# Optimization experiments

Hardware: AMD Instinct MI355X
Metric: run time of the kernel (lower is better)

Reference implementation:

```python
import jax, jax.numpy as jnp
import numpy as np

NP_, NA_, NS_ = 4096, 4096, 1
E_ = 131072
DIN, DOUT, H = 256, 64, 4
SLOPE = 0.2  # leaky relu negative slope


def _leaky(x):
    return jnp.where(x >= 0, x, SLOPE * x)


def setup_inputs() -> dict:
    key = jax.random.key(0)
    ks = iter(jax.random.split(key, 64))
    inp = {}
    inp['feat_P'] = jax.random.normal(next(ks), (NP_, DIN), jnp.float32)
    inp['feat_A'] = jax.random.normal(next(ks), (NA_, DIN), jnp.float32)
    inp['feat_state'] = jax.random.normal(next(ks), (NS_, DIN), jnp.float32)
    for name in ['P', 'A', 'p2p', 'p2a', 'a2p', 'a2a', 'p2s', 'a2s', 'in']:
        inp['W_' + name] = jax.random.normal(next(ks), (DOUT * H, DIN), jnp.float32) / np.sqrt(DIN)
        inp['b_' + name] = jax.random.normal(next(ks), (DOUT * H,), jnp.float32) * 0.01
    for name in ['p2p', 'p2a', 'a2p', 'a2a', 'p2s', 'a2s']:
        inp['att_%s_src' % name] = jax.random.normal(next(ks), (1, H, DOUT), jnp.float32) * 0.1
        inp['att_%s_dst' % name] = jax.random.normal(next(ks), (1, H, DOUT), jnp.float32) * 0.1
    for name, ns, nd in [('p2p', NP_, NP_), ('p2a', NP_, NA_), ('a2p', NA_, NP_), ('a2a', NA_, NA_)]:
        inp['e_%s_src' % name] = jax.random.randint(next(ks), (E_,), 0, ns, jnp.int32)
        inp['e_%s_dst' % name] = jax.random.randint(next(ks), (E_,), 0, nd, jnp.int32)
    inp['e_p2s_src'] = jnp.arange(NP_, dtype=jnp.int32)
    inp['e_p2s_dst'] = jnp.zeros((NP_,), jnp.int32)
    inp['e_a2s_src'] = jnp.arange(NA_, dtype=jnp.int32)
    inp['e_a2s_dst'] = jnp.zeros((NA_,), jnp.int32)
    return inp


def _msg_agg(feat_src, W, b, att_s, att_d, Wh_dst, src, dst, n_dst):
    # per-edge lossy_u_mul_e with comm_loss == 0 (noise branch dead):
    # gather src features, per-edge linear, per-edge softmax over HEADS (torch Softmax(dim=1)).
    h = feat_src[src]                                    # [E, DIN]
    Wh = (h @ W.T + b).reshape(-1, H, DOUT)              # [E, H, D]
    a_s = jnp.sum(Wh * att_s, axis=-1, keepdims=True)    # [E, H, 1]
    a_d = jnp.sum(Wh_dst[dst] * att_d, axis=-1, keepdims=True)
    attn = jax.nn.softmax(_leaky(a_s + a_d), axis=1)     # softmax over heads, as in original
    return jax.ops.segment_sum(Wh * attn, dst, num_segments=n_dst)


def _edge_softmax_agg(Wh_src, att_s, Wh_state, att_d, src, dst, n_dst):
    # dgl edge_softmax: destination-grouped stable softmax over incoming edges.
    a_s = jnp.sum(Wh_src * att_s, axis=-1, keepdims=True)[src]    # [E, H, 1]
    a_d = jnp.sum(Wh_state * att_d, axis=-1, keepdims=True)[dst]  # [E, H, 1]
    e = _leaky(a_s + a_d)
    m = jax.ops.segment_max(e, dst, num_segments=n_dst)
    ex = jnp.exp(e - m[dst])
    den = jax.ops.segment_sum(ex, dst, num_segments=n_dst)
    a = ex / den[dst]
    return jax.ops.segment_sum(Wh_src[src] * a, dst, num_segments=n_dst)


def reference(feat_P, feat_A, feat_state,
              W_P, b_P, W_A, b_A, W_p2p, b_p2p, W_p2a, b_p2a, W_a2p, b_a2p,
              W_a2a, b_a2a, W_p2s, b_p2s, W_a2s, b_a2s, W_in, b_in,
              att_p2p_src, att_p2p_dst, att_p2a_src, att_p2a_dst,
              att_a2p_src, att_a2p_dst, att_a2a_src, att_a2a_dst,
              att_p2s_src, att_p2s_dst, att_a2s_src, att_a2s_dst,
              e_p2p_src, e_p2p_dst, e_p2a_src, e_p2a_dst,
              e_a2p_src, e_a2p_dst, e_a2a_src, e_a2a_dst,
              e_p2s_src, e_p2s_dst, e_a2s_src, e_a2s_dst):
    Whp = (feat_P @ W_P.T + b_P).reshape(NP_, H, DOUT)
    Wha = (feat_A @ W_A.T + b_A).reshape(NA_, H, DOUT)
    Whp2s = (feat_P @ W_p2s.T + b_p2s).reshape(NP_, H, DOUT)
    Wha2s = (feat_A @ W_a2s.T + b_a2s).reshape(NA_, H, DOUT)
    Whin = (feat_state @ W_in.T + b_in).reshape(NS_, H, DOUT)

    ft_p2p = _msg_agg(feat_P, W_p2p, b_p2p, att_p2p_src, att_p2p_dst, Whp, e_p2p_src, e_p2p_dst, NP_)
    ft_p2a = _msg_agg(feat_P, W_p2a, b_p2a, att_p2a_src, att_p2a_dst, Wha, e_p2a_src, e_p2a_dst, NA_)
    ft_a2p = _msg_agg(feat_A, W_a2p, b_a2p, att_a2p_src, att_a2p_dst, Whp, e_a2p_src, e_a2p_dst, NP_)
    ft_a2a = _msg_agg(feat_A, W_a2a, b_a2a, att_a2a_src, att_a2a_dst, Wha, e_a2a_src, e_a2a_dst, NA_)

    ft_p2s = _edge_softmax_agg(Whp2s, att_p2s_src, Whin, att_p2s_dst, e_p2s_src, e_p2s_dst, NS_)
    ft_a2s = _edge_softmax_agg(Wha2s, att_a2s_src, Whin, att_a2s_dst, e_a2s_src, e_a2s_dst, NS_)

    h_P = jax.nn.relu(Whp + ft_p2p + ft_a2p)
    h_A = jax.nn.relu(Wha + ft_p2a + ft_a2a)
    h_S = jax.nn.relu(Whin + ft_p2s + ft_a2s)
    return (h_P, h_A, h_S)
```

## Files before the change

kernel.cpp:

```cpp
#include <hip/hip_runtime.h>

#define NPA   4096
#define DHD   256
#define EDG   131072
#define OS    4104
#define PST   64
#define TBL_SZ ((size_t)NPA * DHD)

#define B_AH    ((size_t)0)
#define B_WH    (B_AH + 2 * TBL_SZ * 2)
#define B_TBL   (B_WH + (size_t)8 * 65536 * 2)
#define B_SCORE (B_TBL + 8 * TBL_SZ * 2)
#define B_CNTP  (B_SCORE + (size_t)10 * NPA * 4 * 4)
#define B_OFFS  (B_CNTP + (size_t)32 * NPA * 4)
#define B_CUR   (B_OFFS + (size_t)4 * OS * 4)
#define B_PKT   (B_CUR + (size_t)4 * NPA * 4)
#define B_WHIN  (B_PKT + (size_t)4 * EDG * 16)
#define B_SCD   (B_WHIN + 256 * 4)
#define B_NUMP  (B_SCD + 8 * 4)
#define B_DENP  (B_NUMP + (size_t)2 * PST * 256 * 4)

typedef _Float16 half8 __attribute__((ext_vector_type(8)));
typedef _Float16 half4 __attribute__((ext_vector_type(4)));
typedef _Float16 half2v __attribute__((ext_vector_type(2)));
typedef float floatx4 __attribute__((ext_vector_type(4)));

struct CastArgs { const float* src[10]; };
struct GemmArgs {
    const float* b[8];
    const float* att0[8]; const float* att1[8];
    int sj0[8]; int sj1[8];
};
struct EdgeArgs { const int* src[4]; const int* dst[4]; };

__device__ __forceinline__ float lrelu(float x) { return x >= 0.0f ? x : 0.2f * x; }

__device__ __forceinline__ int pack2(float a, float b) {
    half2v h = {(_Float16)a, (_Float16)b};
    return __builtin_bit_cast(int, h);
}
__device__ __forceinline__ half2v bc2(int v) { return __builtin_bit_cast(half2v, v); }

__device__ __forceinline__ half2v asplat(const int4& p, int head) {
    int w = (head & 2) ? p.z : p.y;
    int b = (head & 1) ? ((w >> 16) & 0xffff) : (w & 0xffff);
    return bc2(b | (b << 16));
}

__global__ __launch_bounds__(256) void prep_kernel(CastArgs ca, EdgeArgs ea,
        const float* __restrict__ fs, const float* __restrict__ Win,
        const float* __restrict__ bin, const float* __restrict__ attP,
        const float* __restrict__ attA, _Float16* __restrict__ dst,
        int* __restrict__ cntp, float* __restrict__ whin, float* __restrict__ scd) {
    __shared__ int hist[NPA];
    int bid = blockIdx.x;
    int tid = threadIdx.x;
    if (bid < 32) {
        int r = bid >> 3;
        int chunk = bid & 7;
        const int* dp = ea.dst[r] + chunk * 16384;
#pragma unroll
        for (int i = 0; i < 16; ++i) hist[tid + i * 256] = 0;
        __syncthreads();
#pragma unroll
        for (int k = 0; k < 64; ++k)
            atomicAdd(&hist[dp[k * 256 + tid]], 1);
        __syncthreads();
        int* cr = cntp + (size_t)bid * NPA;
#pragma unroll
        for (int i = 0; i < 16; ++i)
            cr[tid + i * 256] = hist[tid + i * 256];
        return;
    }
    if (bid == 32) {
        float* sf = (float*)hist;
        sf[tid] = fs[tid];
        __syncthreads();
        const float* wr = Win + (size_t)tid * 256;
        float acc = bin[tid];
        for (int k = 0; k < 256; k += 4) {
            float4 wv = *(const float4*)(wr + k);
            acc += wv.x * sf[k] + wv.y * sf[k + 1] + wv.z * sf[k + 2] + wv.w * sf[k + 3];
        }
        whin[tid] = acc;
        float v1 = acc * attP[tid];
        float v2 = acc * attA[tid];
        for (int d = 32; d; d >>= 1) { v1 += __shfl_xor(v1, d); v2 += __shfl_xor(v2, d); }
        if ((tid & 63) == 0) { scd[tid >> 6] = v1; scd[4 + (tid >> 6)] = v2; }
        return;
    }
    size_t i4 = ((size_t)(bid - 33) * 256 + tid) * 4;
    const float* s; size_t off;
    if (i4 < TBL_SZ)            { s = ca.src[0]; off = i4; }
    else if (i4 < 2 * TBL_SZ)   { s = ca.src[1]; off = i4 - TBL_SZ; }
    else { size_t r = i4 - 2 * TBL_SZ; s = ca.src[2 + (r >> 16)]; off = r & 65535; }
    float4 v = *(const float4*)(s + off);
    half4 hh = {(_Float16)v.x, (_Float16)v.y, (_Float16)v.z, (_Float16)v.w};
    *(half4*)(dst + i4) = hh;
}

__global__ __launch_bounds__(256) void gemm_scan(const _Float16* __restrict__ Ah,
        const _Float16* __restrict__ Whb, GemmArgs ga, const int* __restrict__ cntp,
        _Float16* __restrict__ tblBase, float* __restrict__ score,
        int* __restrict__ offs, int* __restrict__ cur) {
    int bid = blockIdx.x;
    int t = threadIdx.x;
    if (bid < 4) {
        int r = bid;
        int4 s[4];
#pragma unroll
        for (int q = 0; q < 4; ++q) {
            int4 acc = {0, 0, 0, 0};
#pragma unroll
            for (int b = 0; b < 8; ++b) {
                const int4* cp = (const int4*)(cntp + (size_t)(r * 8 + b) * NPA);
                int4 u = cp[t * 4 + q];
                acc.x += u.x; acc.y += u.y; acc.z += u.z; acc.w += u.w;
            }
            s[q] = acc;
        }
        int lsum = 0;
#pragma unroll
        for (int q = 0; q < 4; ++q) lsum += s[q].x + s[q].y + s[q].z + s[q].w;
        int wave = t >> 6, lane = t & 63;
        int sc = lsum;
#pragma unroll
        for (int d = 1; d < 64; d <<= 1) {
            int u = __shfl_up(sc, d);
            if (lane >= d) sc += u;
        }
        __shared__ int ws4[4];
        if (lane == 63) ws4[wave] = sc;
        __syncthreads();
        int wb = 0;
        for (int w = 0; w < 4; ++w) if (w < wave) wb += ws4[w];
        int run = wb + sc - lsum;
        int* of = offs + (size_t)r * OS;
        int* cu = cur + (size_t)r * NPA;
#pragma unroll
        for (int q = 0; q < 4; ++q) {
            int4 o;
            o.x = run; run += s[q].x;
            o.y = run; run += s[q].y;
            o.z = run; run += s[q].z;
            o.w = run; run += s[q].w;
            ((int4*)of)[t * 4 + q] = o;
            ((int4*)cu)[t * 4 + q] = o;
        }
        if (t == 255) of[NPA] = run;
        return;
    }
    int g = bid - 4;
    int j = g >> 7;
    int mt = g & 127;
    int w = t >> 6, lane = t & 63;
    int quad = lane >> 4, l16 = lane & 15;
    const _Float16* A = Ah + (size_t)(j >> 2) * TBL_SZ;
    const _Float16* W = Whb + (size_t)j * 65536;
    const float* bias = ga.b[j];
    _Float16* out = tblBase + (size_t)j * TBL_SZ;
    int mr0 = mt * 32;
    int nc0 = w * 64;
    const _Float16* ap[2];
    const _Float16* bp[4];
#pragma unroll
    for (int g2 = 0; g2 < 2; ++g2)
        ap[g2] = A + (size_t)(mr0 + g2 * 16 + l16) * 256 + quad * 8;
#pragma unroll
    for (int g2 = 0; g2 < 4; ++g2)
        bp[g2] = W + (size_t)(nc0 + g2 * 16 + l16) * 256 + quad * 8;
    floatx4 acc[2][4];
#pragma unroll
    for (int rg = 0; rg < 2; ++rg)
#pragma unroll
        for (int cg = 0; cg < 4; ++cg) acc[rg][cg] = (floatx4){0, 0, 0, 0};
#pragma unroll
    for (int k0 = 0; k0 < 256; k0 += 32) {
        half8 av[2], bv[4];
#pragma unroll
        for (int g2 = 0; g2 < 2; ++g2) av[g2] = *(const half8*)(ap[g2] + k0);
#pragma unroll
        for (int g2 = 0; g2 < 4; ++g2) bv[g2] = *(const half8*)(bp[g2] + k0);
#pragma unroll
        for (int rg = 0; rg < 2; ++rg)
#pragma unroll
            for (int cg = 0; cg < 4; ++cg)
                acc[rg][cg] = __builtin_amdgcn_mfma_f32_16x16x32_f16(av[rg], bv[cg], acc[rg][cg], 0, 0, 0);
    }
    float bc[4];
#pragma unroll
    for (int cg = 0; cg < 4; ++cg) bc[cg] = bias[nc0 + cg * 16 + l16];
#pragma unroll
    for (int rg = 0; rg < 2; ++rg)
#pragma unroll
        for (int i = 0; i < 4; ++i) {
            int row = mr0 + rg * 16 + quad * 4 + i;
#pragma unroll
            for (int cg = 0; cg < 4; ++cg)
                out[(size_t)row * 256 + nc0 + cg * 16 + l16] = (_Float16)(acc[rg][cg][i] + bc[cg]);
        }
#pragma unroll
    for (int tt = 0; tt < 2; ++tt) {
        const float* att = tt ? ga.att1[j] : ga.att0[j];
        int sj = tt ? ga.sj1[j] : ga.sj0[j];
        if (!att) continue;
        float at[4];
#pragma unroll
        for (int cg = 0; cg < 4; ++cg) at[cg] = att[nc0 + cg * 16 + l16];
        float* sb = score + (size_t)sj * NPA * 4;
#pragma unroll
        for (int rg = 0; rg < 2; ++rg)
#pragma unroll
            for (int i = 0; i < 4; ++i) {
                float p = (acc[rg][0][i] + bc[0]) * at[0] + (acc[rg][1][i] + bc[1]) * at[1]
                        + (acc[rg][2][i] + bc[2]) * at[2] + (acc[rg][3][i] + bc[3]) * at[3];
                p += __shfl_xor(p, 1); p += __shfl_xor(p, 2);
                p += __shfl_xor(p, 4); p += __shfl_xor(p, 8);
                if (l16 == 0) {
                    int row = mr0 + rg * 16 + quad * 4 + i;
                    sb[(size_t)row * 4 + w] = p;
                }
            }
    }
}

__global__ __launch_bounds__(256) void scatter_state(EdgeArgs ea,
        const float* __restrict__ score, int* __restrict__ cur, int4* __restrict__ pkt,
        const _Float16* __restrict__ tblBase, const float* __restrict__ scd,
        float* __restrict__ numP, float* __restrict__ denP) {
    int bid = blockIdx.x;
    int t = threadIdx.x;
    if (bid >= 2048) {
        int sb = bid - 2048;
        int r = sb >> 6;
        int blk = sb & 63;
        int h = t >> 6;
        const _Float16* wh = tblBase + (size_t)(r == 0 ? 3 : 7) * TBL_SZ;
        const float* as = score + (size_t)(8 + r) * NPA * 4;
        float dh = scd[r * 4 + h];
        float dsum = 0.0f, acc = 0.0f;
        for (int i = blk; i < NPA; i += PST) {
            float x = lrelu(as[(size_t)i * 4 + h] + dh);
            float w = __expf(x);
            dsum += w;
            acc += w * (float)wh[(size_t)i * 256 + t];
        }
        numP[(size_t)(r * PST + blk) * 256 + t] = acc;
        if ((t & 63) == 0) denP[(size_t)(r * PST + blk) * 4 + h] = dsum;
        return;
    }
    int idx = bid * 256 + t;
    int r = idx >> 17;
    int e = idx & (EDG - 1);
    int s = ea.src[r][e];
    int d = ea.dst[r][e];
    const float* as = score + (size_t)r * NPA * 4;
    const float* ad = score + (size_t)(4 + r) * NPA * 4;
    float4 av = *(const float4*)&as[(size_t)s * 4];
    float4 dv = *(const float4*)&ad[(size_t)d * 4];
    float x0 = lrelu(av.x + dv.x), x1 = lrelu(av.y + dv.y);
    float x2 = lrelu(av.z + dv.z), x3 = lrelu(av.w + dv.w);
    float m = fmaxf(fmaxf(x0, x1), fmaxf(x2, x3));
    float e0 = __expf(x0 - m), e1 = __expf(x1 - m), e2 = __expf(x2 - m), e3 = __expf(x3 - m);
    float inv = 1.0f / (e0 + e1 + e2 + e3);
    int pos = atomicAdd(&cur[r * NPA + d], 1);
    int4 pk = {s, pack2(e0 * inv, e1 * inv), pack2(e2 * inv, e3 * inv), 0};
    pkt[(size_t)r * EDG + pos] = pk;
}

__global__ __launch_bounds__(256) void agg_final(const int* __restrict__ offs,
        const int4* __restrict__ pkt, const _Float16* __restrict__ tblBase,
        const float* __restrict__ whin, const float* __restrict__ numP,
        const float* __restrict__ denP, float* __restrict__ outBase) {
    int bid = blockIdx.x;
    int tid = threadIdx.x;
    if (bid == 2048) {
        int t = tid;
        int h = t >> 6;
        float n0 = 0.f, n1 = 0.f, d0 = 0.f, d1 = 0.f;
        for (int b = 0; b < PST; ++b) {
            n0 += numP[(size_t)b * 256 + t];
            n1 += numP[(size_t)(PST + b) * 256 + t];
            d0 += denP[(size_t)b * 4 + h];
            d1 += denP[(size_t)(PST + b) * 4 + h];
        }
        float v = whin[t] + n0 / d0 + n1 / d1;
        outBase[2 * TBL_SZ + t] = fmaxf(v, 0.f);
        return;
    }
    int side = bid >> 10;
    int bx = bid & 1023;
    int wave = tid >> 6, lane = tid & 63;
    int dn = bx * 4 + wave;
    int h = lane >> 5, l32 = lane & 31;
    int head = l32 >> 3;
    half2v accA[4] = {{0,0},{0,0},{0,0},{0,0}};
    half2v accB[4] = {{0,0},{0,0},{0,0},{0,0}};
    const int srcIdx[4] = {1, 2, 5, 6};
    const int4 z = {0, 0, 0, 0};
#pragma unroll
    for (int q = 0; q < 2; ++q) {
        int r = side + q * 2;
        const int* of = offs + (size_t)r * OS;
        const int4* pkb = pkt + (size_t)r * EDG;
        const _Float16* wh = tblBase + (size_t)srcIdx[r] * TBL_SZ;
        int beg = of[dn], end = of[dn + 1];
        int i = beg;
        int4 p0 = (i + h     < end) ? pkb[i + h]     : z;
        int4 p1 = (i + 2 + h < end) ? pkb[i + 2 + h] : z;
        int4 p2 = (i + 4 + h < end) ? pkb[i + 4 + h] : z;
        int4 p3 = (i + 6 + h < end) ? pkb[i + 6 + h] : z;
        while (i < end) {
            int ni = i + 8;
            half8 w0 = *(const half8*)(wh + (size_t)p0.x * 256 + l32 * 8);
            half8 w1 = *(const half8*)(wh + (size_t)p1.x * 256 + l32 * 8);
            half8 w2 = *(const half8*)(wh + (size_t)p2.x * 256 + l32 * 8);
            half8 w3 = *(const half8*)(wh + (size_t)p3.x * 256 + l32 * 8);
            int4 n0 = (ni + h     < end) ? pkb[ni + h]     : z;
            int4 n1 = (ni + 2 + h < end) ? pkb[ni + 2 + h] : z;
            int4 n2 = (ni + 4 + h < end) ? pkb[ni + 4 + h] : z;
            int4 n3 = (ni + 6 + h < end) ? pkb[ni + 6 + h] : z;
            half2v a0 = asplat(p0, head), a1 = asplat(p1, head);
            half2v a2 = asplat(p2, head), a3 = asplat(p3, head);
            int4 i0 = __builtin_bit_cast(int4, w0);
            int4 i1 = __builtin_bit_cast(int4, w1);
            int4 i2 = __builtin_bit_cast(int4, w2);
            int4 i3 = __builtin_bit_cast(int4, w3);
            accA[0] += bc2(i0.x) * a0; accA[1] += bc2(i0.y) * a0;
            accA[2] += bc2(i0.z) * a0; accA[3] += bc2(i0.w) * a0;
            accB[0] += bc2(i1.x) * a1; accB[1] += bc2(i1.y) * a1;
            accB[2] += bc2(i1.z) * a1; accB[3] += bc2(i1.w) * a1;
            accA[0] += bc2(i2.x) * a2; accA[1] += bc2(i2.y) * a2;
            accA[2] += bc2(i2.z) * a2; accA[3] += bc2(i2.w) * a2;
            accB[0] += bc2(i3.x) * a3; accB[1] += bc2(i3.y) * a3;
            accB[2] += bc2(i3.z) * a3; accB[3] += bc2(i3.w) * a3;
            p0 = n0; p1 = n1; p2 = n2; p3 = n3;
            i = ni;
        }
    }
    float f[8];
#pragma unroll
    for (int k = 0; k < 4; ++k) {
        half2v s = accA[k] + accB[k];
        f[2 * k] = (float)s[0];
        f[2 * k + 1] = (float)s[1];
    }
#pragma unroll
    for (int k = 0; k < 8; ++k) f[k] += __shfl_xor(f[k], 32);
    if (h == 0) {
        const _Float16* skip = tblBase + (size_t)(side * 4) * TBL_SZ + (size_t)dn * 256 + l32 * 8;
        half8 sv = *(const half8*)skip;
        float* op = outBase + ((size_t)side * NPA + dn) * 256 + l32 * 8;
        float4 o0 = {fmaxf(f[0] + (float)sv[0], 0.f), fmaxf(f[1] + (float)sv[1], 0.f),
                     fmaxf(f[2] + (float)sv[2], 0.f), fmaxf(f[3] + (float)sv[3], 0.f)};
        float4 o1 = {fmaxf(f[4] + (float)sv[4], 0.f), fmaxf(f[5] + (float)sv[5], 0.f),
                     fmaxf(f[6] + (float)sv[6], 0.f), fmaxf(f[7] + (float)sv[7], 0.f)};
        *(float4*)op = o0;
        *(float4*)(op + 4) = o1;
    }
}

extern "C" void kernel_launch(void* const* d_in, const int* in_sizes, int n_in,
                              void* d_out, int out_size, void* d_ws, size_t ws_size,
                              hipStream_t stream) {
    auto F = [&](int i) { return (const float*)d_in[i]; };
    char* ws = (char*)d_ws;
    _Float16* Ah  = (_Float16*)(ws + B_AH);
    _Float16* Whb = (_Float16*)(ws + B_WH);
    _Float16* tbl = (_Float16*)(ws + B_TBL);
    float* score  = (float*)(ws + B_SCORE);
    int* cntp     = (int*)(ws + B_CNTP);
    int* offs     = (int*)(ws + B_OFFS);
    int* cur      = (int*)(ws + B_CUR);
    int4* pkt     = (int4*)(ws + B_PKT);
    float* whin   = (float*)(ws + B_WHIN);
    float* scd    = (float*)(ws + B_SCD);
    float* numP   = (float*)(ws + B_NUMP);
    float* denP   = (float*)(ws + B_DENP);

    CastArgs ca = {{F(0), F(1), F(3), F(7), F(9), F(15), F(5), F(11), F(13), F(17)}};
    EdgeArgs ea = {{(const int*)d_in[33], (const int*)d_in[35], (const int*)d_in[37], (const int*)d_in[39]},
                   {(const int*)d_in[34], (const int*)d_in[36], (const int*)d_in[38], (const int*)d_in[40]}};

    prep_kernel<<<2593, 256, 0, stream>>>(ca, ea, F(2), F(19), F(20), F(30), F(32),
                                          Ah, cntp, whin, scd);

    GemmArgs ga;
    const int bIdx[8] = {4, 8, 10, 16, 6, 12, 14, 18};
    for (int j = 0; j < 8; ++j) ga.b[j] = F(bIdx[j]);
    const int a0Idx[8]  = {22, 21, 23, 29, 24, 25, 27, 31};
    const int sj0Arr[8] = { 4,  0,  1,  8,  5,  2,  3,  9};
    for (int j = 0; j < 8; ++j) {
        ga.att0[j] = F(a0Idx[j]); ga.sj0[j] = sj0Arr[j];
        ga.att1[j] = nullptr;     ga.sj1[j] = -1;
    }
    ga.att1[0] = F(26); ga.sj1[0] = 6;
    ga.att1[4] = F(28); ga.sj1[4] = 7;

    gemm_scan<<<4 + 1024, 256, 0, stream>>>(Ah, Whb, ga, cntp, tbl, score, offs, cur);
    scatter_state<<<2048 + 2 * PST, 256, 0, stream>>>(ea, score, cur, pkt, tbl, scd, numP, denP);
    agg_final<<<2049, 256, 0, stream>>>(offs, pkt, tbl, whin, numP, denP, (float*)d_out);
}
```

Measured before the change: 269.4 us.

## Replace global atomic bucket cursor with per-chunk LDS cursors in CSR scatter

The edge histogram is now built per 4096-edge chunk (32 chunks per relation). The scan kernel computes a per-chunk base offset for every destination node. The scatter kernel then runs one block per chunk, loads those bases into shared memory and uses LDS atomics to claim packet slots, in place of global atomics on a shared cursor array. This removes contended global atomics but makes the scan blocks walk 32 chunk histograms twice, with more serial work, and cuts the scatter grid from 2048 to 128 blocks.

```diff
diff --git a/kernel.cpp b/kernel.cpp
--- a/kernel.cpp
+++ b/kernel.cpp
@@ -5,6 +5,7 @@
 #define EDG   131072
 #define OS    4104
 #define PST   64
+#define NCH   32
 #define TBL_SZ ((size_t)NPA * DHD)
 
 #define B_AH    ((size_t)0)
@@ -12,9 +13,9 @@
 #define B_TBL   (B_WH + (size_t)8 * 65536 * 2)
 #define B_SCORE (B_TBL + 8 * TBL_SZ * 2)
 #define B_CNTP  (B_SCORE + (size_t)10 * NPA * 4 * 4)
-#define B_OFFS  (B_CNTP + (size_t)32 * NPA * 4)
-#define B_CUR   (B_OFFS + (size_t)4 * OS * 4)
-#define B_PKT   (B_CUR + (size_t)4 * NPA * 4)
+#define B_CBASE (B_CNTP + (size_t)4 * NCH * NPA * 4)
+#define B_OFFS  (B_CBASE + (size_t)4 * NCH * NPA * 4)
+#define B_PKT   (B_OFFS + (size_t)4 * OS * 4)
 #define B_WHIN  (B_PKT + (size_t)4 * EDG * 16)
 #define B_SCD   (B_WHIN + 256 * 4)
 #define B_NUMP  (B_SCD + 8 * 4)
@@ -55,15 +56,15 @@
     __shared__ int hist[NPA];
     int bid = blockIdx.x;
     int tid = threadIdx.x;
-    if (bid < 32) {
-        int r = bid >> 3;
-        int chunk = bid & 7;
-        const int* dp = ea.dst[r] + chunk * 16384;
+    if (bid < 128) {
+        int r = bid >> 5;
+        int c = bid & 31;
+        const int* dp = ea.dst[r] + c * 4096;
 #pragma unroll
         for (int i = 0; i < 16; ++i) hist[tid + i * 256] = 0;
         __syncthreads();
 #pragma unroll
-        for (int k = 0; k < 64; ++k)
+        for (int k = 0; k < 16; ++k)
             atomicAdd(&hist[dp[k * 256 + tid]], 1);
         __syncthreads();
         int* cr = cntp + (size_t)bid * NPA;
@@ -72,7 +73,7 @@
             cr[tid + i * 256] = hist[tid + i * 256];
         return;
     }
-    if (bid == 32) {
+    if (bid == 128) {
         float* sf = (float*)hist;
         sf[tid] = fs[tid];
         __syncthreads();
@@ -89,7 +90,7 @@
         if ((tid & 63) == 0) { scd[tid >> 6] = v1; scd[4 + (tid >> 6)] = v2; }
         return;
     }
-    size_t i4 = ((size_t)(bid - 33) * 256 + tid) * 4;
+    size_t i4 = ((size_t)(bid - 129) * 256 + tid) * 4;
     const float* s; size_t off;
     if (i4 < TBL_SZ)            { s = ca.src[0]; off = i4; }
     else if (i4 < 2 * TBL_SZ)   { s = ca.src[1]; off = i4 - TBL_SZ; }
@@ -102,19 +103,18 @@
 __global__ __launch_bounds__(256) void gemm_scan(const _Float16* __restrict__ Ah,
         const _Float16* __restrict__ Whb, GemmArgs ga, const int* __restrict__ cntp,
         _Float16* __restrict__ tblBase, float* __restrict__ score,
-        int* __restrict__ offs, int* __restrict__ cur) {
+        int* __restrict__ offs, int* __restrict__ cbase) {
     int bid = blockIdx.x;
     int t = threadIdx.x;
     if (bid < 4) {
         int r = bid;
+        const int4* cpr = (const int4*)(cntp + (size_t)r * NCH * NPA);
         int4 s[4];
 #pragma unroll
         for (int q = 0; q < 4; ++q) {
             int4 acc = {0, 0, 0, 0};
-#pragma unroll
-            for (int b = 0; b < 8; ++b) {
-                const int4* cp = (const int4*)(cntp + (size_t)(r * 8 + b) * NPA);
-                int4 u = cp[t * 4 + q];
+            for (int c = 0; c < NCH; ++c) {
+                int4 u = cpr[(size_t)c * (NPA / 4) + t * 4 + q];
                 acc.x += u.x; acc.y += u.y; acc.z += u.z; acc.w += u.w;
             }
             s[q] = acc;
@@ -136,7 +136,7 @@
         for (int w = 0; w < 4; ++w) if (w < wave) wb += ws4[w];
         int run = wb + sc - lsum;
         int* of = offs + (size_t)r * OS;
-        int* cu = cur + (size_t)r * NPA;
+        int4 ob[4];
 #pragma unroll
         for (int q = 0; q < 4; ++q) {
             int4 o;
@@ -145,9 +145,19 @@
             o.z = run; run += s[q].z;
             o.w = run; run += s[q].w;
             ((int4*)of)[t * 4 + q] = o;
-            ((int4*)cu)[t * 4 + q] = o;
+            ob[q] = o;
         }
         if (t == 255) of[NPA] = run;
+        int4* cbr = (int4*)(cbase + (size_t)r * NCH * NPA);
+#pragma unroll
+        for (int q = 0; q < 4; ++q) {
+            int4 running = ob[q];
+            for (int c = 0; c < NCH; ++c) {
+                cbr[(size_t)c * (NPA / 4) + t * 4 + q] = running;
+                int4 u = cpr[(size_t)c * (NPA / 4) + t * 4 + q];
+                running.x += u.x; running.y += u.y; running.z += u.z; running.w += u.w;
+            }
+        }
         return;
     }
     int g = bid - 4;
@@ -225,13 +235,14 @@
 }
 
 __global__ __launch_bounds__(256) void scatter_state(EdgeArgs ea,
-        const float* __restrict__ score, int* __restrict__ cur, int4* __restrict__ pkt,
+        const float* __restrict__ score, const int* __restrict__ cbase, int4* __restrict__ pkt,
         const _Float16* __restrict__ tblBase, const float* __restrict__ scd,
         float* __restrict__ numP, float* __restrict__ denP) {
+    __shared__ int lpos[NPA];
     int bid = blockIdx.x;
     int t = threadIdx.x;
-    if (bid >= 2048) {
-        int sb = bid - 2048;
+    if (bid >= 128) {
+        int sb = bid - 128;
         int r = sb >> 6;
         int blk = sb & 63;
         int h = t >> 6;
@@ -249,23 +260,33 @@
         if ((t & 63) == 0) denP[(size_t)(r * PST + blk) * 4 + h] = dsum;
         return;
     }
-    int idx = bid * 256 + t;
-    int r = idx >> 17;
-    int e = idx & (EDG - 1);
-    int s = ea.src[r][e];
-    int d = ea.dst[r][e];
+    int r = bid >> 5;
+    int c = bid & 31;
+    const int* cb = cbase + (size_t)(r * NCH + c) * NPA;
+#pragma unroll
+    for (int i = 0; i < 16; ++i) lpos[t + i * 256] = cb[t + i * 256];
+    __syncthreads();
+    const int* sp = ea.src[r] + c * 4096;
+    const int* dp = ea.dst[r] + c * 4096;
     const float* as = score + (size_t)r * NPA * 4;
     const float* ad = score + (size_t)(4 + r) * NPA * 4;
-    float4 av = *(const float4*)&as[(size_t)s * 4];
-    float4 dv = *(const float4*)&ad[(size_t)d * 4];
-    float x0 = lrelu(av.x + dv.x), x1 = lrelu(av.y + dv.y);
-    float x2 = lrelu(av.z + dv.z), x3 = lrelu(av.w + dv.w);
-    float m = fmaxf(fmaxf(x0, x1), fmaxf(x2, x3));
-    float e0 = __expf(x0 - m), e1 = __expf(x1 - m), e2 = __expf(x2 - m), e3 = __expf(x3 - m);
-    float inv = 1.0f / (e0 + e1 + e2 + e3);
-    int pos = atomicAdd(&cur[r * NPA + d], 1);
-    int4 pk = {s, pack2(e0 * inv, e1 * inv), pack2(e2 * inv, e3 * inv), 0};
-    pkt[(size_t)r * EDG + pos] = pk;
+    int4* pkb = pkt + (size_t)r * EDG;
+#pragma unroll 4
+    for (int k = 0; k < 16; ++k) {
+        int e = k * 256 + t;
+        int s = sp[e];
+        int d = dp[e];
+        float4 av = *(const float4*)&as[(size_t)s * 4];
+        float4 dv = *(const float4*)&ad[(size_t)d * 4];
+        float x0 = lrelu(av.x + dv.x), x1 = lrelu(av.y + dv.y);
+        float x2 = lrelu(av.z + dv.z), x3 = lrelu(av.w + dv.w);
+        float m = fmaxf(fmaxf(x0, x1), fmaxf(x2, x3));
+        float e0 = __expf(x0 - m), e1 = __expf(x1 - m), e2 = __expf(x2 - m), e3 = __expf(x3 - m);
+        float inv = 1.0f / (e0 + e1 + e2 + e3);
+        int pos = atomicAdd(&lpos[d], 1);
+        int4 pk = {s, pack2(e0 * inv, e1 * inv), pack2(e2 * inv, e3 * inv), 0};
+        pkb[pos] = pk;
+    }
 }
 
 __global__ __launch_bounds__(256) void agg_final(const int* __restrict__ offs,
@@ -370,8 +391,8 @@
     _Float16* tbl = (_Float16*)(ws + B_TBL);
     float* score  = (float*)(ws + B_SCORE);
     int* cntp     = (int*)(ws + B_CNTP);
+    int* cbase    = (int*)(ws + B_CBASE);
     int* offs     = (int*)(ws + B_OFFS);
-    int* cur      = (int*)(ws + B_CUR);
     int4* pkt     = (int4*)(ws + B_PKT);
     float* whin   = (float*)(ws + B_WHIN);
     float* scd    = (float*)(ws + B_SCD);
@@ -382,7 +403,7 @@
     EdgeArgs ea = {{(const int*)d_in[33], (const int*)d_in[35], (const int*)d_in[37], (const int*)d_in[39]},
                    {(const int*)d_in[34], (const int*)d_in[36], (const int*)d_in[38], (const int*)d_in[40]}};
 
-    prep_kernel<<<2593, 256, 0, stream>>>(ca, ea, F(2), F(19), F(20), F(30), F(32),
+    prep_kernel<<<2689, 256, 0, stream>>>(ca, ea, F(2), F(19), F(20), F(30), F(32),
                                           Ah, cntp, whin, scd);
 
     GemmArgs ga;
@@ -397,7 +418,7 @@
     ga.att1[0] = F(26); ga.sj1[0] = 6;
     ga.att1[4] = F(28); ga.sj1[4] = 7;
 
-    gemm_scan<<<4 + 1024, 256, 0, stream>>>(Ah, Whb, ga, cntp, tbl, score, offs, cur);
-    scatter_state<<<2048 + 2 * PST, 256, 0, stream>>>(ea, score, cur, pkt, tbl, scd, numP, denP);
+    gemm_scan<<<4 + 1024, 256, 0, stream>>>(Ah, Whb, ga, cntp, tbl, score, offs, cbase);
+    scatter_state<<<128 + 2 * PST, 256, 0, stream>>>(ea, score, cbase, pkt, tbl, scd, numP, denP);
     agg_final<<<2049, 256, 0, stream>>>(offs, pkt, tbl, whin, numP, denP, (float*)d_out);
 }
```

Measured after the change: 247.0 us. 1.09x faster.
